# Kernel optimization log

Hardware: AMD Instinct MI355X
Metric: run time of the kernel (lower is better)

The kernel has to match this reference:

```python
import jax, jax.numpy as jnp
import numpy as np


def setup_inputs() -> dict:
    key = jax.random.key(0)
    k1, k2, k3, k4 = jax.random.split(key, 4)
    B, T, IN, D = 32, 256, 64, 128
    x = jax.random.normal(k1, (B, T, IN), dtype=jnp.float32)
    h0 = jnp.zeros((B, D), dtype=jnp.float32)
    Wx = jax.random.normal(k2, (IN, D), dtype=jnp.float32) * 0.01
    Wgate = jax.random.normal(k3, (D, D), dtype=jnp.float32) * 0.01
    Wh = jax.random.normal(k4, (D, D), dtype=jnp.float32) * 0.01
    return {"x": x, "h0": h0, "Wx": Wx, "Wgate": Wgate, "Wh": Wh}


def reference(x, h0, Wx, Wgate, Wh):
    # x: (B, T, in_dim); h0: (B, dim); returns (h_final, y, hidden_grads, dh_dWh)
    def step_single(h_r, x_r):
        # per-sample gated update: h_r (dim,), x_r (in_dim,)
        pre = x_r @ Wx + h_r @ Wh
        a = jax.nn.gelu(pre, approximate=False)  # torch GELU() is the exact erf variant
        g = jax.nn.sigmoid(a @ Wgate)
        hn = g * h_r + (1.0 - g)
        return hn, hn

    # per-step, per-sample Jacobian d h_new / d h  (mirrors vmap(jacrev(..., argnums=1)))
    jac_batched = jax.vmap(jax.jacrev(step_single, argnums=0, has_aux=True))

    def body(h, x_t):  # h: (B, dim), x_t: (B, in_dim)
        jac, h_new = jac_batched(h, x_t)  # jac: (B, dim, dim)
        return h_new, (h_new, jac)

    xt = jnp.swapaxes(x, 0, 1)  # (T, B, in_dim)
    h_final, (ys, jacs) = jax.lax.scan(body, h0, xt)
    y = jnp.swapaxes(ys, 0, 1)  # (B, T, dim)

    # last-step Jacobian wrt Wh, evaluated with the post-update h (as in the torch code)
    x_last = x[:, -1, :]

    def f_wh(Wh_):
        pre = x_last @ Wx + h_final @ Wh_
        a = jax.nn.gelu(pre, approximate=False)
        g = jax.nn.sigmoid(a @ Wgate)
        return g * h_final + (1.0 - g)

    dh_dWh = jax.jacrev(f_wh)(Wh)  # (B, dim, dim, dim)
    return (h_final, y, jacs, dh_dWh)
```

## Files before the change

kernel.cpp:

```cpp
#include <hip/hip_runtime.h>


#define JACOFF 1052672L
#define DHWOFF 135270400L

typedef __attribute__((ext_vector_type(8))) short frag_ab;
typedef __attribute__((ext_vector_type(4))) float frag_cd;

__device__ __forceinline__ short f2bf(float f) {
    unsigned u = __builtin_bit_cast(unsigned, f);
    unsigned r = (u + 0x7fffu + ((u >> 16) & 1u)) >> 16;
    return (short)r;
}

__device__ __forceinline__ void wg_barrier() {
    asm volatile("s_waitcnt lgkmcnt(0)\n\ts_barrier" ::: "memory");
}

__device__ __forceinline__ float row_reduce16(float x) {
    int t;
    t = __builtin_amdgcn_mov_dpp(__builtin_bit_cast(int, x), 0x128, 0xF, 0xF, true);
    x += __builtin_bit_cast(float, t);
    t = __builtin_amdgcn_mov_dpp(__builtin_bit_cast(int, x), 0x124, 0xF, 0xF, true);
    x += __builtin_bit_cast(float, t);
    t = __builtin_amdgcn_mov_dpp(__builtin_bit_cast(int, x), 0x4E, 0xF, 0xF, true);
    x += __builtin_bit_cast(float, t);
    t = __builtin_amdgcn_mov_dpp(__builtin_bit_cast(int, x), 0xB1, 0xF, 0xF, true);
    x += __builtin_bit_cast(float, t);
    return x;
}

__device__ __forceinline__ void gelu_pair(float pre, float& a, float& dval) {
    const float inv_sqrt2   = 0.70710678118654752f;
    const float inv_sqrt2pi = 0.39894228040143268f;
    float ex2 = __expf(-0.5f * pre * pre);
    float az  = fabsf(pre) * inv_sqrt2;
    float t   = 1.0f / (1.0f + 0.3275911f * az);
    float poly = ((((1.061405429f * t - 1.453152027f) * t + 1.421413741f) * t
                   - 0.284496736f) * t + 0.254829592f) * t;
    float erf_abs = 1.0f - poly * ex2;
    float erf_z = (pre < 0.f) ? -erf_abs : erf_abs;
    float cdf = 0.5f * (1.0f + erf_z);
    a = pre * cdf;
    dval = cdf + pre * inv_sqrt2pi * ex2;
}

__global__ __launch_bounds__(256) void prep_xw_kernel(
    const float* __restrict__ Wh, const float* __restrict__ Wg,
    const float* __restrict__ x, const float* __restrict__ Wx,
    float* __restrict__ whT, float* __restrict__ wgT, float* __restrict__ xw)
{
    int blk = blockIdx.x;
    int tid = threadIdx.x;
    if (blk < 128) {
        int idx = blk * 256 + tid;
        if (idx < 16384) {
            int k = idx >> 7, i = idx & 127;
            whT[i * 128 + k] = Wh[idx];
        } else {
            int r = idx - 16384;
            int k = r >> 7, i = r & 127;
            wgT[i * 128 + k] = Wg[r];
        }
        return;
    }
    __shared__ float xs[2][64];
    int sub = tid >> 7;
    int bt = (blk - 128) * 2 + sub;
    int i = tid & 127;
    if (i < 64) xs[sub][i] = x[bt * 64 + i];
    __syncthreads();
    float acc = 0.f;
#pragma unroll
    for (int m = 0; m < 64; ++m)
        acc += xs[sub][m] * Wx[m * 128 + i];
    xw[bt * 128 + i] = acc;
}

__global__ __launch_bounds__(512, 1) void scan_pk_kernel(
    const float* __restrict__ xw, const float* __restrict__ h0,
    const float* __restrict__ whT, const float* __restrict__ wgT,
    const float* __restrict__ Wgate, const float* __restrict__ Wh,
    float* __restrict__ out,
    short* __restrict__ Abf, float* __restrict__ wgv, float* __restrict__ wc,
    float* __restrict__ wdF, float* __restrict__ wuF, float* __restrict__ whF,
    short* __restrict__ PT)
{
    int tid = threadIdx.x;
    if (blockIdx.x >= 32) {
        int c = (blockIdx.x - 32) * 32 + (tid >> 4);
        int k0 = (tid & 15) * 8;
        int i = c >> 7, j = c & 127;
        short v[8];
#pragma unroll
        for (int m = 0; m < 8; ++m) {
            float wg = Wgate[(k0 + m) * 128 + i];
            float wh = Wh[j * 128 + k0 + m];
            v[m] = f2bf(wg * wh);
        }
        *(frag_ab*)(PT + (long)c * 128 + k0) = *(frag_ab*)v;
        return;
    }

    const int b = blockIdx.x;
    const int og = tid >> 4;
    const int kg = tid & 15;
    const int mm = kg & 3;
    const int iw = og * 4 + kg;
    const bool wlane = (kg < 4);

    __shared__ float hbuf[2][128];
    __shared__ float abuf[128];

    float wh[4][8], wgc[4][8];
#pragma unroll
    for (int m = 0; m < 4; ++m) {
        const float* whr = whT + (og * 4 + m) * 128 + kg * 8;
        const float* wgr = wgT + (og * 4 + m) * 128 + kg * 8;
        float4 a4 = *(const float4*)(whr);
        float4 b4 = *(const float4*)(whr + 4);
        wh[m][0] = a4.x; wh[m][1] = a4.y; wh[m][2] = a4.z; wh[m][3] = a4.w;
        wh[m][4] = b4.x; wh[m][5] = b4.y; wh[m][6] = b4.z; wh[m][7] = b4.w;
        float4 c4 = *(const float4*)(wgr);
        float4 d4 = *(const float4*)(wgr + 4);
        wgc[m][0] = c4.x; wgc[m][1] = c4.y; wgc[m][2] = c4.z; wgc[m][3] = c4.w;
        wgc[m][4] = d4.x; wgc[m][5] = d4.y; wgc[m][6] = d4.z; wgc[m][7] = d4.w;
    }
    if (wlane) hbuf[0][iw] = h0[b * 128 + iw];
    __syncthreads();

    float4 xwv4 = *(const float4*)(xw + (b * 256 + 0) * 128 + og * 4);
    float4 xw14 = *(const float4*)(xw + (b * 256 + 1) * 128 + og * 4);

    for (int t = 0; t < 256; ++t) {
        int p = t & 1;
        int tn = (t < 254) ? t + 2 : 255;
        float4 xw24 = *(const float4*)(xw + (b * 256 + tn) * 128 + og * 4);

        float h8[8];
        {
            const float* hb = &hbuf[p][kg * 8];
            float4 a4 = *(const float4*)(hb);
            float4 b4 = *(const float4*)(hb + 4);
            h8[0] = a4.x; h8[1] = a4.y; h8[2] = a4.z; h8[3] = a4.w;
            h8[4] = b4.x; h8[5] = b4.y; h8[6] = b4.z; h8[7] = b4.w;
        }
        float s0 = 0.f, s1 = 0.f, s2 = 0.f, s3 = 0.f;
#pragma unroll
        for (int kk = 0; kk < 8; ++kk) {
            s0 += h8[kk] * wh[0][kk];
            s1 += h8[kk] * wh[1][kk];
            s2 += h8[kk] * wh[2][kk];
            s3 += h8[kk] * wh[3][kk];
        }
        s0 = row_reduce16(s0); s1 = row_reduce16(s1);
        s2 = row_reduce16(s2); s3 = row_reduce16(s3);

        float pre = (mm == 0) ? (xwv4.x + s0) : (mm == 1) ? (xwv4.y + s1)
                  : (mm == 2) ? (xwv4.z + s2) : (xwv4.w + s3);
        float a, dval;
        gelu_pair(pre, a, dval);

        long tb = (long)(t * 32 + b) * 128 + iw;
        if (wlane) {
            Abf[tb] = f2bf(dval);
            abuf[iw] = a;
        }
        wg_barrier();

        float a8[8];
        {
            const float* ab = &abuf[kg * 8];
            float4 a4 = *(const float4*)(ab);
            float4 b4 = *(const float4*)(ab + 4);
            a8[0] = a4.x; a8[1] = a4.y; a8[2] = a4.z; a8[3] = a4.w;
            a8[4] = b4.x; a8[5] = b4.y; a8[6] = b4.z; a8[7] = b4.w;
        }
        float r0 = 0.f, r1 = 0.f, r2 = 0.f, r3 = 0.f;
#pragma unroll
        for (int kk = 0; kk < 8; ++kk) {
            r0 += a8[kk] * wgc[0][kk];
            r1 += a8[kk] * wgc[1][kk];
            r2 += a8[kk] * wgc[2][kk];
            r3 += a8[kk] * wgc[3][kk];
        }
        r0 = row_reduce16(r0); r1 = row_reduce16(r1);
        r2 = row_reduce16(r2); r3 = row_reduce16(r3);
        float r = (mm == 0) ? r0 : (mm == 1) ? r1 : (mm == 2) ? r2 : r3;

        float g = 1.0f / (1.0f + __expf(-r));
        float hp = hbuf[p][og * 4 + mm];
        float c = (hp - 1.0f) * g * (1.0f - g);
        float hn = g * hp + 1.0f - g;
        if (wlane) {
            hbuf[p ^ 1][iw] = hn;
            wgv[tb] = g;
            wc[tb] = c;
            out[4096 + (b * 256 + t) * 128 + iw] = hn;
        }
        xwv4 = xw14; xw14 = xw24;
        wg_barrier();
    }

    float hfin = hbuf[0][og * 4 + mm];
    if (wlane) {
        out[b * 128 + iw] = hbuf[0][iw];
        whF[b * 128 + iw] = hbuf[0][iw];
    }

    {
        float h8[8];
        {
            const float* hb = &hbuf[0][kg * 8];
            float4 a4 = *(const float4*)(hb);
            float4 b4 = *(const float4*)(hb + 4);
            h8[0] = a4.x; h8[1] = a4.y; h8[2] = a4.z; h8[3] = a4.w;
            h8[4] = b4.x; h8[5] = b4.y; h8[6] = b4.z; h8[7] = b4.w;
        }
        float s0 = 0.f, s1 = 0.f, s2 = 0.f, s3 = 0.f;
#pragma unroll
        for (int kk = 0; kk < 8; ++kk) {
            s0 += h8[kk] * wh[0][kk];
            s1 += h8[kk] * wh[1][kk];
            s2 += h8[kk] * wh[2][kk];
            s3 += h8[kk] * wh[3][kk];
        }
        s0 = row_reduce16(s0); s1 = row_reduce16(s1);
        s2 = row_reduce16(s2); s3 = row_reduce16(s3);
        float pre = (mm == 0) ? (xwv4.x + s0) : (mm == 1) ? (xwv4.y + s1)
                  : (mm == 2) ? (xwv4.z + s2) : (xwv4.w + s3);
        float a, dval;
        gelu_pair(pre, a, dval);
        if (wlane) {
            wdF[b * 128 + iw] = dval;
            abuf[iw] = a;
        }
        __syncthreads();
        float a8[8];
        {
            const float* ab = &abuf[kg * 8];
            float4 a4 = *(const float4*)(ab);
            float4 b4 = *(const float4*)(ab + 4);
            a8[0] = a4.x; a8[1] = a4.y; a8[2] = a4.z; a8[3] = a4.w;
            a8[4] = b4.x; a8[5] = b4.y; a8[6] = b4.z; a8[7] = b4.w;
        }
        float r0 = 0.f, r1 = 0.f, r2 = 0.f, r3 = 0.f;
#pragma unroll
        for (int kk = 0; kk < 8; ++kk) {
            r0 += a8[kk] * wgc[0][kk];
            r1 += a8[kk] * wgc[1][kk];
            r2 += a8[kk] * wgc[2][kk];
            r3 += a8[kk] * wgc[3][kk];
        }
        r0 = row_reduce16(r0); r1 = row_reduce16(r1);
        r2 = row_reduce16(r2); r3 = row_reduce16(r3);
        float r = (mm == 0) ? r0 : (mm == 1) ? r1 : (mm == 2) ? r2 : r3;
        float g = 1.0f / (1.0f + __expf(-r));
        if (wlane) wuF[b * 128 + iw] = (hfin - 1.0f) * g * (1.0f - g);
    }
}

__global__ __launch_bounds__(256) void jacmm_dhdw_kernel(
    const short* __restrict__ Abf,
    const short* __restrict__ PT,
    const float* __restrict__ wgv,
    const float* __restrict__ wc,
    const float* __restrict__ Wgate,
    const float* __restrict__ dF, const float* __restrict__ uF, const float* __restrict__ hF,
    float* __restrict__ out)
{
    int bx = blockIdx.x;
    int tid = threadIdx.x;
    int grp = bx / 3, rem = bx % 3;

    if (rem == 2) {
        __shared__ float hs[128], dsh[128];
        int b = grp >> 7, i = grp & 127;
        if (tid < 128) {
            hs[tid] = hF[b * 128 + tid];
            dsh[tid] = dF[b * 128 + tid];
        }
        __syncthreads();
        float u = uF[b * 128 + i];
        int q0 = (tid & 31) * 4, p0 = (tid >> 5) * 16;
        float w0 = u * dsh[q0 + 0] * Wgate[(q0 + 0) * 128 + i];
        float w1 = u * dsh[q0 + 1] * Wgate[(q0 + 1) * 128 + i];
        float w2 = u * dsh[q0 + 2] * Wgate[(q0 + 2) * 128 + i];
        float w3 = u * dsh[q0 + 3] * Wgate[(q0 + 3) * 128 + i];
        float* dst = out + DHWOFF + (long)grp * 16384;
#pragma unroll
        for (int pp = 0; pp < 16; ++pp) {
            float hp = hs[p0 + pp];
            *(float4*)(dst + (p0 + pp) * 128 + q0) = make_float4(hp * w0, hp * w1, hp * w2, hp * w3);
        }
        return;
    }

    int jb = grp * 2 + rem;
    int rb = jb & 63;
    int cb = jb >> 6;

    const short* Ag = Abf + (long)rb * (128 * 128);
    const short* Bg = PT + (long)cb * (128 * 128);

    int w = tid >> 6;
    int lane = tid & 63;
    int wr = w >> 1;
    int wcol = w & 1;
    int lrow = lane & 15;
    int quad = lane >> 4;

    long rowbase = (long)rb * 128;
    float ci[4][4], gi[4][4];
#pragma unroll
    for (int p = 0; p < 4; ++p) {
        int trow0 = wr * 64 + p * 16 + quad * 4;
#pragma unroll
        for (int reg = 0; reg < 4; ++reg) {
            long row = rowbase + trow0 + reg;
            ci[p][reg] = wc[row * 128 + cb];
            gi[p][reg] = wgv[row * 128 + cb];
        }
    }

    frag_cd acc[4][4];
#pragma unroll
    for (int p = 0; p < 4; ++p)
#pragma unroll
        for (int q = 0; q < 4; ++q) {
            acc[p][q][0] = 0.f; acc[p][q][1] = 0.f; acc[p][q][2] = 0.f; acc[p][q][3] = 0.f;
        }

#pragma unroll
    for (int kk = 0; kk < 4; ++kk) {
        int ko8 = (kk * 4 + quad) * 8;
        frag_ab af[4], bf[4];
#pragma unroll
        for (int p = 0; p < 4; ++p) {
            int r = wr * 64 + p * 16 + lrow;
            af[p] = *(const frag_ab*)(Ag + r * 128 + ko8);
        }
#pragma unroll
        for (int q = 0; q < 4; ++q) {
            int n = wcol * 64 + q * 16 + lrow;
            bf[q] = *(const frag_ab*)(Bg + n * 128 + ko8);
        }
#pragma unroll
        for (int p = 0; p < 4; ++p)
#pragma unroll
            for (int q = 0; q < 4; ++q)
                acc[p][q] = __builtin_amdgcn_mfma_f32_16x16x32_bf16(af[p], bf[q], acc[p][q], 0, 0, 0);
    }

#pragma unroll
    for (int p = 0; p < 4; ++p) {
        int trow0 = wr * 64 + p * 16 + quad * 4;
#pragma unroll
        for (int reg = 0; reg < 4; ++reg) {
            long row = rowbase + trow0 + reg;
            float* orow = out + JACOFF + row * 16384 + (long)cb * 128;
#pragma unroll
            for (int q = 0; q < 4; ++q) {
                int tcol = wcol * 64 + q * 16 + lrow;
                float v = ci[p][reg] * acc[p][q][reg];
                if (tcol == cb) v += gi[p][reg];
                orow[tcol] = v;
            }
        }
    }
}

extern "C" void kernel_launch(void* const* d_in, const int* in_sizes, int n_in,
                              void* d_out, int out_size, void* d_ws, size_t ws_size,
                              hipStream_t stream)
{
    (void)in_sizes; (void)n_in; (void)out_size; (void)ws_size;
    const float* x     = (const float*)d_in[0];
    const float* h0    = (const float*)d_in[1];
    const float* Wx    = (const float*)d_in[2];
    const float* Wgate = (const float*)d_in[3];
    const float* Wh    = (const float*)d_in[4];
    float* out = (float*)d_out;
    float* ws  = (float*)d_ws;

    float* xw  = ws;
    float* whT = ws + 1048576;
    float* wgT = ws + 1064960;
    float* wgv = ws + 1081344;
    float* wc  = ws + 2129920;
    float* wdF = ws + 3178496;
    float* wuF = ws + 3182592;
    float* whF = ws + 3186688;
    short* Abf = (short*)(ws + 3190784);
    short* PT  = (short*)(ws + 3715072);

    prep_xw_kernel<<<4224, 256, 0, stream>>>(Wh, Wgate, x, Wx, whT, wgT, xw);
    scan_pk_kernel<<<544, 512, 0, stream>>>(xw, h0, whT, wgT, Wgate, Wh, out,
                                            Abf, wgv, wc, wdF, wuF, whF, PT);
    jacmm_dhdw_kernel<<<12288, 256, 0, stream>>>(Abf, PT, wgv, wc, Wgate, wdF, wuF, whF, out);
}
```

Measured before the change: 1.096 ms.

## Stage Jacobian tiles through LDS for coalesced float4 nontemporal stores

The MFMA epilogue now writes the scaled accumulator tile into a padded shared-memory buffer in two halves, then reads it back so each thread emits contiguous float4 rows. This replaces scattered scalar global stores with coalesced 16-byte writes. Both the Jacobian output and the dh/dWh outer-product output now use nontemporal stores to avoid cache pollution on the large write-only outputs. It adds extra barriers and about 33KB of LDS per block, which may lower occupancy.

```diff
diff --git a/kernel.cpp b/kernel.cpp
--- a/kernel.cpp
+++ b/kernel.cpp
@@ -273,6 +273,8 @@
     int tid = threadIdx.x;
     int grp = bx / 3, rem = bx % 3;
 
+    __shared__ float cstage[64 * 132];
+
     if (rem == 2) {
         __shared__ float hs[128], dsh[128];
         int b = grp >> 7, i = grp & 127;
@@ -291,7 +293,8 @@
 #pragma unroll
         for (int pp = 0; pp < 16; ++pp) {
             float hp = hs[p0 + pp];
-            *(float4*)(dst + (p0 + pp) * 128 + q0) = make_float4(hp * w0, hp * w1, hp * w2, hp * w3);
+            frag_cd v4; v4[0] = hp * w0; v4[1] = hp * w1; v4[2] = hp * w2; v4[3] = hp * w3;
+            __builtin_nontemporal_store(v4, (frag_cd*)(dst + (p0 + pp) * 128 + q0));
         }
         return;
     }
@@ -353,19 +356,34 @@
     }
 
 #pragma unroll
-    for (int p = 0; p < 4; ++p) {
-        int trow0 = wr * 64 + p * 16 + quad * 4;
-#pragma unroll
-        for (int reg = 0; reg < 4; ++reg) {
-            long row = rowbase + trow0 + reg;
-            float* orow = out + JACOFF + row * 16384 + (long)cb * 128;
-#pragma unroll
-            for (int q = 0; q < 4; ++q) {
-                int tcol = wcol * 64 + q * 16 + lrow;
-                float v = ci[p][reg] * acc[p][q][reg];
-                if (tcol == cb) v += gi[p][reg];
-                orow[tcol] = v;
+    for (int p0 = 0; p0 < 4; p0 += 2) {
+        if (p0) __syncthreads();
+#pragma unroll
+        for (int dp = 0; dp < 2; ++dp) {
+            int p = p0 + dp;
+#pragma unroll
+            for (int reg = 0; reg < 4; ++reg) {
+                int lr = wr * 32 + dp * 16 + quad * 4 + reg;
+                float cval = ci[p][reg], gval = gi[p][reg];
+#pragma unroll
+                for (int q = 0; q < 4; ++q) {
+                    int tcol = wcol * 64 + q * 16 + lrow;
+                    float v = cval * acc[p][q][reg];
+                    if (tcol == cb) v += gval;
+                    cstage[lr * 132 + tcol] = v;
+                }
             }
+        }
+        __syncthreads();
+        int col4 = (tid & 31) * 4;
+        int rg = tid >> 5;
+#pragma unroll
+        for (int rr = 0; rr < 8; ++rr) {
+            int lr = rg * 8 + rr;
+            int grow = (lr < 32) ? (p0 * 16 + lr) : (64 + p0 * 16 + (lr - 32));
+            frag_cd v4 = *(const frag_cd*)&cstage[lr * 132 + col4];
+            __builtin_nontemporal_store(
+                v4, (frag_cd*)(out + JACOFF + (rowbase + grow) * 16384 + (long)cb * 128 + col4));
         }
     }
 }
```

New measurement: 1.046 ms. -4.6%, faster.
